# Optimization experiments

Hardware: AMD Instinct MI355X
Metric: run time of the kernel (lower is better)

Reference implementation:

```python
import jax, jax.numpy as jnp
import numpy as np

B, T, D, H, K, V, W = 2, 2048, 1024, 16, 64, 64, 256
BANK = 64
CUE = 50250
EPS = 1e-6
SCALE = K ** -0.5
LOCAL_SCALE = 0.3
ROPE_BASE = 10000.0


def setup_inputs() -> dict:
    key = jax.random.key(0)
    ks = jax.random.split(key, 13)
    s = 0.02
    return {
        "x": jax.random.normal(ks[0], (B, T, D), jnp.float32),
        "gdn_state": jax.random.normal(ks[1], (B, H, K, V), jnp.float32),
        "input_ids": jax.random.randint(ks[2], (B, T), 0, 50320),
        "key_bank": jax.random.normal(ks[3], (H, BANK, K), jnp.float32),
        "norm_w": jnp.ones((D,), jnp.float32),
        "wq": jax.random.normal(ks[4], (D, D), jnp.float32) * s,
        "wk": jax.random.normal(ks[5], (D, D), jnp.float32) * s,
        "wv": jax.random.normal(ks[6], (D, D), jnp.float32) * s,
        "wo": jax.random.normal(ks[7], (D, D), jnp.float32) * s,
        "w_gq": jax.random.normal(ks[8], (H * K, D), jnp.float32) * s,
        "w_ro": jax.random.normal(ks[9], (D, H * V), jnp.float32) * s,
        "w_gate": jax.random.normal(ks[10], (H, D), jnp.float32) * s,
        "b_gate": jnp.ones((H,), jnp.float32),
    }


def _rope(u):
    # u: [B, T, H, K]
    inv_freq = 1.0 / (ROPE_BASE ** (jnp.arange(0, K, 2, dtype=jnp.float32) / K))
    t = jnp.arange(T, dtype=jnp.float32)
    freqs = t[:, None] * inv_freq[None, :]            # [T, K/2]
    emb = jnp.concatenate([freqs, freqs], axis=-1)    # [T, K]
    cos = jnp.cos(emb)[None, :, None, :]
    sin = jnp.sin(emb)[None, :, None, :]
    u1, u2 = u[..., : K // 2], u[..., K // 2 :]
    rotated = jnp.concatenate([-u2, u1], axis=-1)
    return u * cos + rotated * sin


def reference(x, gdn_state, input_ids, key_bank, norm_w, wq, wk, wv, wo,
              w_gq, w_ro, w_gate, b_gate):
    # RMSNorm
    rms = jnp.sqrt(jnp.mean(x * x, axis=-1, keepdims=True) + EPS)
    x_norm = x / rms * norm_w

    # QKV projections -> [B, T, H, K]
    q = (x_norm @ wq.T).reshape(B, T, H, K)
    k = (x_norm @ wk.T).reshape(B, T, H, K)
    v = (x_norm @ wv.T).reshape(B, T, H, K)
    q = _rope(q)
    k = _rope(k)

    # Causal sliding-window attention (PyTorch fallback math: full TxT + band mask)
    scores = jnp.einsum("bthk,bshk->bhts", q, k) * SCALE  # [B, H, T, T]
    i = jnp.arange(T)
    allowed = (i[None, :] <= i[:, None]) & (i[None, :] >= i[:, None] - W)  # [T, T]
    scores = jnp.where(allowed[None, None], scores, jnp.float32(-jnp.inf))
    probs = jax.nn.softmax(scores, axis=-1)
    local = jnp.einsum("bhts,bshv->bthv", probs, v).reshape(B, T, D)
    local = LOCAL_SCALE * (local @ wo.T)  # eval path: local_scale * o_proj(local_out)

    # Global retrieval from GDN state
    q_g = (x_norm @ w_gq.T).reshape(B, T, H, K)
    # CUE token override: positions with input_ids == CUE + idx use key_bank[:, idx, :]
    idx = input_ids - CUE                              # [B, T]
    valid = (idx >= 0) & (idx < BANK)
    ci = jnp.clip(idx, 0, BANK - 1)
    gathered = key_bank.transpose(1, 0, 2)[ci]         # [B, T, H, K]
    q_g = jnp.where(valid[..., None, None], gathered, q_g)

    retrieved = jnp.einsum("bhkv,bthk->bthv", gdn_state, q_g).reshape(B, T, H * V)
    retrieval_out = retrieved @ w_ro.T                 # [B, T, D]
    gate = jax.nn.sigmoid(x_norm @ w_gate.T + b_gate)  # [B, T, H]
    retrieval_out = jnp.mean(gate, axis=-1, keepdims=True) * retrieval_out

    return x + local + retrieval_out
```

## Files before the change

kernel.cpp:

```cpp
#include <hip/hip_runtime.h>
#include <cstddef>

typedef __bf16 bf16_t;
typedef __bf16 bf16x8 __attribute__((ext_vector_type(8)));
typedef __bf16 bf16x4 __attribute__((ext_vector_type(4)));
typedef float  f32x4  __attribute__((ext_vector_type(4)));

struct CvtArgs { const float* s[6]; bf16_t* d[6]; float scale[6]; };
__global__ __launch_bounds__(256) void prep_kernel(CvtArgs ca,
                                                   const float* __restrict__ x,
                                                   const float* __restrict__ nw,
                                                   const float* __restrict__ wg,
                                                   const float* __restrict__ bg,
                                                   bf16_t* __restrict__ xn,
                                                   float* __restrict__ gm,
                                                   float2* __restrict__ rtab,
                                                   float* __restrict__ dout) {
  __shared__ float red[4];
  __shared__ float gred[4][16];
  int bid = blockIdx.x;
  int tid = threadIdx.x;
  if (bid < 6144) {
    int m = bid >> 10;
    int i = (bid & 1023) * 256 + tid;
    f32x4 v = ((const f32x4*)ca.s[m])[i];
    float sc = ca.scale[m];
    bf16x4 o;
    #pragma unroll
    for (int j = 0; j < 4; ++j) o[j] = (bf16_t)(v[j] * sc);
    *(bf16x4*)(ca.d[m] + (size_t)i * 4) = o;
    return;
  }
  if (bid < 6400) {
    int i = (bid - 6144) * 256 + tid;
    int t = i >> 5, d = i & 31;
    float inv = exp2f((float)d * -0.41524101186092029f);
    float sn, cs;
    sincosf((float)t * inv, &sn, &cs);
    rtab[i] = make_float2(cs, sn);
    return;
  }
  int t = bid - 6400;
  int wave = tid >> 6, lane = tid & 63;
  f32x4 v = ((const f32x4*)(x + (size_t)t * 1024))[tid];
  ((f32x4*)(dout + (size_t)t * 1024))[tid] = v;
  float ss = v[0]*v[0] + v[1]*v[1] + v[2]*v[2] + v[3]*v[3];
  #pragma unroll
  for (int off = 32; off >= 1; off >>= 1) ss += __shfl_xor(ss, off);
  if (lane == 0) red[wave] = ss;
  __syncthreads();
  float tot = red[0] + red[1] + red[2] + red[3];
  float rinv = rsqrtf(tot * (1.0f / 1024.0f) + 1e-6f);
  f32x4 wv = ((const f32x4*)nw)[tid];
  float xnv[4];
  bf16x4 o;
  #pragma unroll
  for (int i = 0; i < 4; ++i) { xnv[i] = v[i] * rinv * wv[i]; o[i] = (bf16_t)xnv[i]; }
  *(bf16x4*)(xn + (size_t)t * 1024 + tid * 4) = o;
  float ga[16];
  #pragma unroll
  for (int h = 0; h < 16; ++h) {
    f32x4 wgh = ((const f32x4*)(wg + h * 1024))[tid];
    ga[h] = xnv[0]*wgh[0] + xnv[1]*wgh[1] + xnv[2]*wgh[2] + xnv[3]*wgh[3];
  }
  #pragma unroll
  for (int h = 0; h < 16; ++h) {
    #pragma unroll
    for (int off = 32; off >= 1; off >>= 1) ga[h] += __shfl_xor(ga[h], off);
  }
  if (lane < 16) gred[wave][lane] = ga[lane];
  __syncthreads();
  if (tid < 16) {
    float s = gred[0][tid] + gred[1][tid] + gred[2][tid] + gred[3][tid];
    float sig = 1.0f / (1.0f + __expf(-(s + bg[tid])));
    #pragma unroll
    for (int off = 8; off >= 1; off >>= 1) sig += __shfl_xor(sig, off);
    if (tid == 0) gm[t] = sig * (1.0f / 16.0f);
  }
}

struct GemmSeg { const bf16_t* a; const bf16_t* w; void* c; int mode; };
struct GemmCfg { GemmSeg seg[4]; const float2* rope; };
#define LDSK 40
template<int KD>
__global__ __launch_bounds__(256, 2) void gemm_bt(GemmCfg cfg) {
  __shared__ bf16_t As[128 * LDSK];
  __shared__ bf16_t Bs[128 * LDSK];
  int seg = blockIdx.x >> 3;
  const bf16_t* __restrict__ A = cfg.seg[seg].a;
  const bf16_t* __restrict__ W = cfg.seg[seg].w;
  int m0 = blockIdx.y * 128;
  int n0 = (blockIdx.x & 7) * 128;
  int tid = threadIdx.x;
  int lane = tid & 63, wave = tid >> 6;
  int wm = (wave >> 1) * 64, wn = (wave & 1) * 64;
  int l16 = lane & 15, quad = lane >> 4;
  f32x4 acc[4][4] = {};
  for (int k0 = 0; k0 < KD; k0 += 32) {
    __syncthreads();
    #pragma unroll
    for (int c = 0; c < 2; ++c) {
      int ci = tid + c * 256;
      int r = ci >> 2;
      int ko = (ci & 3) * 8;
      *(uint4*)&As[r * LDSK + ko] = *(const uint4*)&A[(size_t)(m0 + r) * KD + k0 + ko];
      *(uint4*)&Bs[r * LDSK + ko] = *(const uint4*)&W[(size_t)(n0 + r) * KD + k0 + ko];
    }
    __syncthreads();
    bf16x8 af[4], bfr[4];
    #pragma unroll
    for (int i = 0; i < 4; ++i) {
      af[i]  = *(const bf16x8*)&As[(wm + i * 16 + l16) * LDSK + quad * 8];
      bfr[i] = *(const bf16x8*)&Bs[(wn + i * 16 + l16) * LDSK + quad * 8];
    }
    #pragma unroll
    for (int i = 0; i < 4; ++i)
      #pragma unroll
      for (int j = 0; j < 4; ++j)
        acc[i][j] = __builtin_amdgcn_mfma_f32_16x16x32_bf16(af[i], bfr[j], acc[i][j], 0, 0, 0);
  }
  int mode = cfg.seg[seg].mode;
  if (mode == 1) {
    const float2* tab = cfg.rope;
    #pragma unroll
    for (int jp = 0; jp < 2; ++jp) {
      int d = jp * 16 + l16;
      #pragma unroll
      for (int i = 0; i < 4; ++i)
        #pragma unroll
        for (int r = 0; r < 4; ++r) {
          int tseq = (m0 + wm + i * 16 + quad * 4 + r) & 2047;
          float2 cz = tab[(tseq << 5) + d];
          float v1 = acc[i][jp][r], v2 = acc[i][jp + 2][r];
          acc[i][jp][r]     = v1 * cz.x - v2 * cz.y;
          acc[i][jp + 2][r] = v2 * cz.x + v1 * cz.y;
        }
    }
  }
  if (mode == 3) {
    float* C = (float*)cfg.seg[seg].c;
    #pragma unroll
    for (int i = 0; i < 4; ++i)
      #pragma unroll
      for (int j = 0; j < 4; ++j) {
        int row = m0 + wm + i * 16 + quad * 4;
        int col = n0 + wn + j * 16 + l16;
        #pragma unroll
        for (int r = 0; r < 4; ++r)
          unsafeAtomicAdd(&C[(size_t)(row + r) * 1024 + col], acc[i][j][r]);
      }
  } else {
    bf16_t* C = (bf16_t*)cfg.seg[seg].c;
    #pragma unroll
    for (int i = 0; i < 4; ++i)
      #pragma unroll
      for (int j = 0; j < 4; ++j) {
        int row = m0 + wm + i * 16 + quad * 4;
        int col = n0 + wn + j * 16 + l16;
        #pragma unroll
        for (int r = 0; r < 4; ++r)
          C[(size_t)(row + r) * 1024 + col] = (bf16_t)acc[i][j][r];
      }
  }
}

__global__ __launch_bounds__(256) void attn_retr(const bf16_t* __restrict__ qb,
                                                 const bf16_t* __restrict__ kb,
                                                 const bf16_t* __restrict__ vb,
                                                 const bf16_t* __restrict__ qgb,
                                                 const int* __restrict__ ids,
                                                 const float* __restrict__ bank,
                                                 const float* __restrict__ gdn,
                                                 const float* __restrict__ gm,
                                                 bf16_t* __restrict__ attn_b,
                                                 bf16_t* __restrict__ retr_b) {
  __shared__ alignas(16) char smem[35840];
  int tid = threadIdx.x;
  if (blockIdx.x < 1024) {
    bf16_t* Ks = (bf16_t*)smem;
    bf16_t* Vt = (bf16_t*)(smem + 9216);
    float*  Oa = (float*)(smem + 18432);
    int blk = blockIdx.x;
    int tcb = blk & 31;
    int h = (blk >> 5) & 15;
    int b = blk >> 9;
    int t0 = tcb * 64;
    int wv = tid >> 6, lane = tid & 63;
    int l15 = lane & 15, quad = lane >> 4;
    int tq0 = t0 + wv * 16;
    int t = tq0 + l15;
    int lo = t - 256; if (lo < 0) lo = 0;

    const bf16_t* qptr = qb + (((size_t)(b * 2048 + t) * 16) + h) * 64;
    bf16x8 qf0 = *(const bf16x8*)(qptr + quad * 8);
    bf16x8 qf1 = *(const bf16x8*)(qptr + 32 + quad * 8);

    f32x4 acc[4] = {};
    float mrun = -1e30f, lrun = 0.f;

    for (int c = 0; c < 5; ++c) {
      int s0 = t0 - 256 + c * 64;
      __syncthreads();
      #pragma unroll
      for (int it = 0; it < 2; ++it) {
        int task = tid + it * 256;
        int key = task >> 3, dseg = task & 7;
        int s = s0 + key; s = s < 0 ? 0 : (s > 2047 ? 2047 : s);
        *(bf16x8*)&Ks[key * 72 + dseg * 8] =
          *(const bf16x8*)(kb + (((size_t)(b * 2048 + s) * 16) + h) * 64 + dseg * 8);
      }
      {
        int vseg = tid & 7, kp = tid >> 3;
        int sA = s0 + 2 * kp, sB = sA + 1;
        sA = sA < 0 ? 0 : (sA > 2047 ? 2047 : sA);
        sB = sB < 0 ? 0 : (sB > 2047 ? 2047 : sB);
        bf16x8 va = *(const bf16x8*)(vb + (((size_t)(b * 2048 + sA) * 16) + h) * 64 + vseg * 8);
        bf16x8 vbv = *(const bf16x8*)(vb + (((size_t)(b * 2048 + sB) * 16) + h) * 64 + vseg * 8);
        #pragma unroll
        for (int j = 0; j < 8; ++j) {
          union { bf16_t h2[2]; unsigned int u; } pk;
          pk.h2[0] = va[j]; pk.h2[1] = vbv[j];
          *(unsigned int*)&Vt[(vseg * 8 + j) * 72 + 2 * kp] = pk.u;
        }
      }
      __syncthreads();
      #pragma unroll
      for (int p = 0; p < 2; ++p) {
        int sbase = s0 + p * 32;
        if (sbase > tq0 + 15 || sbase + 31 < tq0 - 256 || sbase + 31 < 0) continue;
        int kl = p * 32;
        bf16x8 ka0  = *(const bf16x8*)&Ks[(kl + l15) * 72 + quad * 8];
        bf16x8 ka0b = *(const bf16x8*)&Ks[(kl + l15) * 72 + 32 + quad * 8];
        bf16x8 ka1  = *(const bf16x8*)&Ks[(kl + 16 + l15) * 72 + quad * 8];
        bf16x8 ka1b = *(const bf16x8*)&Ks[(kl + 16 + l15) * 72 + 32 + quad * 8];
        f32x4 c0 = {}, c1 = {};
        c0 = __builtin_amdgcn_mfma_f32_16x16x32_bf16(ka0,  qf0, c0, 0, 0, 0);
        c0 = __builtin_amdgcn_mfma_f32_16x16x32_bf16(ka0b, qf1, c0, 0, 0, 0);
        c1 = __builtin_amdgcn_mfma_f32_16x16x32_bf16(ka1,  qf0, c1, 0, 0, 0);
        c1 = __builtin_amdgcn_mfma_f32_16x16x32_bf16(ka1b, qf1, c1, 0, 0, 0);
        float p0[4], p1[4];
        float mx = -1e30f;
        #pragma unroll
        for (int r = 0; r < 4; ++r) {
          int sK0 = sbase + quad * 4 + r;
          int sK1 = sK0 + 16;
          float v0 = (sK0 >= lo && sK0 <= t) ? c0[r] * 0.125f : -1e30f;
          float v1 = (sK1 >= lo && sK1 <= t) ? c1[r] * 0.125f : -1e30f;
          p0[r] = v0; p1[r] = v1;
          mx = fmaxf(mx, fmaxf(v0, v1));
        }
        mx = fmaxf(mx, __shfl_xor(mx, 16));
        mx = fmaxf(mx, __shfl_xor(mx, 32));
        float mnew = fmaxf(mrun, mx);
        float alpha = __expf(mrun - mnew);
        float rs = 0.f;
        #pragma unroll
        for (int r = 0; r < 4; ++r) {
          float e0 = (p0[r] > -1e29f) ? __expf(p0[r] - mnew) : 0.f;
          float e1 = (p1[r] > -1e29f) ? __expf(p1[r] - mnew) : 0.f;
          p0[r] = e0; p1[r] = e1;
          rs += e0 + e1;
        }
        rs += __shfl_xor(rs, 16);
        rs += __shfl_xor(rs, 32);
        mrun = mnew;
        lrun = lrun * alpha + rs;
        #pragma unroll
        for (int vt = 0; vt < 4; ++vt)
          #pragma unroll
          for (int r = 0; r < 4; ++r) acc[vt][r] *= alpha;
        union { bf16x4 v; int2 i2; } pka, pkb;
        #pragma unroll
        for (int r = 0; r < 4; ++r) { pka.v[r] = (bf16_t)p0[r]; pkb.v[r] = (bf16_t)p1[r]; }
        int sel = quad >> 1;
        int base = l15 + ((quad & 1) << 5);
        int a0 = __shfl(pka.i2.x, base),      b0 = __shfl(pkb.i2.x, base);
        int a1 = __shfl(pka.i2.y, base),      b1 = __shfl(pkb.i2.y, base);
        int a2 = __shfl(pka.i2.x, base + 16), b2 = __shfl(pkb.i2.x, base + 16);
        int a3 = __shfl(pka.i2.y, base + 16), b3 = __shfl(pkb.i2.y, base + 16);
        union { int4 i4; bf16x8 v; } pf;
        pf.i4.x = sel ? b0 : a0;
        pf.i4.y = sel ? b1 : a1;
        pf.i4.z = sel ? b2 : a2;
        pf.i4.w = sel ? b3 : a3;
        #pragma unroll
        for (int vt = 0; vt < 4; ++vt) {
          bf16x8 vfr = *(const bf16x8*)&Vt[(vt * 16 + l15) * 72 + kl + quad * 8];
          acc[vt] = __builtin_amdgcn_mfma_f32_16x16x32_bf16(vfr, pf.v, acc[vt], 0, 0, 0);
        }
      }
    }
    float rl = 1.0f / lrun;
    float* myOs = Oa + wv * (16 * 68);
    #pragma unroll
    for (int vt = 0; vt < 4; ++vt)
      #pragma unroll
      for (int r = 0; r < 4; ++r)
        myOs[l15 * 68 + vt * 16 + quad * 4 + r] = acc[vt][r] * rl;
    __syncthreads();
    #pragma unroll
    for (int q = 0; q < 16; ++q) {
      float v = myOs[q * 68 + lane];
      attn_b[(size_t)(b * 2048 + tq0 + q) * 1024 + h * 64 + lane] = (bf16_t)v;
    }
  } else {
    float* G = (float*)smem;
    int blk = blockIdx.x - 1024;
    int tc = blk & 7;
    int h = (blk >> 3) & 15;
    int b = blk >> 7;
    const f32x4* gsrc = (const f32x4*)(gdn + (size_t)(b * 16 + h) * 4096);
    #pragma unroll
    for (int it = 0; it < 4; ++it)
      ((f32x4*)G)[tid + it * 256] = gsrc[tid + it * 256];
    __syncthreads();
    int t = tc * 256 + tid;
    int id = ids[b * 2048 + t] - 50250;
    bool valid = (id >= 0) && (id < 64);
    const bf16_t* qrow = qgb + (((size_t)(b * 2048 + t) * 16) + h) * 64;
    const float* krow = bank + (size_t)(h * 64 + (valid ? id : 0)) * 64;
    float acc[64];
    #pragma unroll
    for (int v = 0; v < 64; ++v) acc[v] = 0.f;
    for (int k = 0; k < 64; ++k) {
      float qv = valid ? krow[k] : (float)qrow[k];
      const f32x4* gr = (const f32x4*)&G[k * 64];
      #pragma unroll
      for (int i = 0; i < 16; ++i) {
        f32x4 gv = gr[i];
        acc[i * 4 + 0] += qv * gv[0];
        acc[i * 4 + 1] += qv * gv[1];
        acc[i * 4 + 2] += qv * gv[2];
        acc[i * 4 + 3] += qv * gv[3];
      }
    }
    float g = gm[b * 2048 + t];
    bf16_t* orow = retr_b + (size_t)(b * 2048 + t) * 1024 + h * 64;
    #pragma unroll
    for (int i = 0; i < 8; ++i) {
      bf16x8 ov;
      #pragma unroll
      for (int j = 0; j < 8; ++j) ov[j] = (bf16_t)(acc[i * 8 + j] * g);
      *(bf16x8*)(orow + i * 8) = ov;
    }
  }
}

extern "C" void kernel_launch(void* const* d_in, const int* in_sizes, int n_in,
                              void* d_out, int out_size, void* d_ws, size_t ws_size,
                              hipStream_t stream) {
  const float* x        = (const float*)d_in[0];
  const float* gdn      = (const float*)d_in[1];
  const int*   ids      = (const int*)d_in[2];
  const float* key_bank = (const float*)d_in[3];
  const float* norm_w   = (const float*)d_in[4];
  const float* wq       = (const float*)d_in[5];
  const float* wk       = (const float*)d_in[6];
  const float* wv       = (const float*)d_in[7];
  const float* wo       = (const float*)d_in[8];
  const float* w_gq     = (const float*)d_in[9];
  const float* w_ro     = (const float*)d_in[10];
  const float* w_gate   = (const float*)d_in[11];
  const float* b_gate   = (const float*)d_in[12];

  char* p = (char*)d_ws;
  auto alloc = [&](size_t bytes) { char* r = p; p += (bytes + 255) & ~(size_t)255; return r; };
  const size_t ACT = (size_t)4096 * 1024 * 2;
  const size_t WTB = (size_t)1024 * 1024 * 2;
  bf16_t* xn_b   = (bf16_t*)alloc(ACT);
  bf16_t* wq_b   = (bf16_t*)alloc(WTB);
  bf16_t* wk_b   = (bf16_t*)alloc(WTB);
  bf16_t* wv_b   = (bf16_t*)alloc(WTB);
  bf16_t* wgq_b  = (bf16_t*)alloc(WTB);
  bf16_t* wo_b   = (bf16_t*)alloc(WTB);
  bf16_t* wro_b  = (bf16_t*)alloc(WTB);
  bf16_t* qb     = (bf16_t*)alloc(ACT);
  bf16_t* kb     = (bf16_t*)alloc(ACT);
  bf16_t* vb     = (bf16_t*)alloc(ACT);
  bf16_t* qgb    = (bf16_t*)alloc(ACT);
  bf16_t* attn_b = (bf16_t*)alloc(ACT);
  bf16_t* retr_b = (bf16_t*)alloc(ACT);
  float*  gmean  = (float*)alloc(4096 * 4);
  float2* rtab   = (float2*)alloc(2048 * 32 * sizeof(float2));

  CvtArgs ca;
  ca.s[0] = wq;   ca.d[0] = wq_b;   ca.scale[0] = 1.0f;
  ca.s[1] = wk;   ca.d[1] = wk_b;   ca.scale[1] = 1.0f;
  ca.s[2] = wv;   ca.d[2] = wv_b;   ca.scale[2] = 1.0f;
  ca.s[3] = w_gq; ca.d[3] = wgq_b;  ca.scale[3] = 1.0f;
  ca.s[4] = wo;   ca.d[4] = wo_b;   ca.scale[4] = 0.3f;
  ca.s[5] = w_ro; ca.d[5] = wro_b;  ca.scale[5] = 1.0f;
  prep_kernel<<<10496, 256, 0, stream>>>(ca, x, norm_w, w_gate, b_gate,
                                         xn_b, gmean, rtab, (float*)d_out);

  GemmCfg g4;
  g4.seg[0] = {xn_b, wq_b,  (void*)qb,  1};
  g4.seg[1] = {xn_b, wk_b,  (void*)kb,  1};
  g4.seg[2] = {xn_b, wv_b,  (void*)vb,  0};
  g4.seg[3] = {xn_b, wgq_b, (void*)qgb, 0};
  g4.rope = rtab;
  gemm_bt<1024><<<dim3(32, 32), 256, 0, stream>>>(g4);

  attn_retr<<<1280, 256, 0, stream>>>(qb, kb, vb, qgb, ids, key_bank, gdn,
                                      gmean, attn_b, retr_b);

  GemmCfg gf;
  gf.seg[0] = {attn_b, wo_b,  d_out, 3};
  gf.seg[1] = {retr_b, wro_b, d_out, 3};
  gf.seg[2] = gf.seg[0];
  gf.seg[3] = gf.seg[0];
  gf.rope = nullptr;
  gemm_bt<1024><<<dim3(16, 32), 256, 0, stream>>>(gf);
}
```

Before: 263.1 us.

## Split-K the output GEMM and widen K tile for the QKV GEMM

Adds a per-segment K offset so the final output projection is split into two K halves per operand, doubling the grid from 512 to 1024 blocks and relying on mode-3 atomic accumulation into the output. The QKV GEMM switches to a 64-wide K tile, halving the number of barrier pairs per K loop at the cost of more LDS per block. The aim is better CU occupancy on the small output GEMM and less sync overhead on the large one. It adds more atomic traffic and LDS pressure in exchange.

```diff
diff --git a/kernel.cpp b/kernel.cpp
--- a/kernel.cpp
+++ b/kernel.cpp
@@ -79,16 +79,18 @@
   }
 }
 
-struct GemmSeg { const bf16_t* a; const bf16_t* w; void* c; int mode; };
+struct GemmSeg { const bf16_t* a; const bf16_t* w; void* c; int mode; int koff; };
 struct GemmCfg { GemmSeg seg[4]; const float2* rope; };
-#define LDSK 40
-template<int KD>
+template<int KD, int KLEN, int BK>
 __global__ __launch_bounds__(256, 2) void gemm_bt(GemmCfg cfg) {
+  constexpr int LDSK = BK + 8;
+  constexpr int KC = BK / 8;
   __shared__ bf16_t As[128 * LDSK];
   __shared__ bf16_t Bs[128 * LDSK];
   int seg = blockIdx.x >> 3;
   const bf16_t* __restrict__ A = cfg.seg[seg].a;
   const bf16_t* __restrict__ W = cfg.seg[seg].w;
+  int koff = cfg.seg[seg].koff;
   int m0 = blockIdx.y * 128;
   int n0 = (blockIdx.x & 7) * 128;
   int tid = threadIdx.x;
@@ -96,28 +98,31 @@
   int wm = (wave >> 1) * 64, wn = (wave & 1) * 64;
   int l16 = lane & 15, quad = lane >> 4;
   f32x4 acc[4][4] = {};
-  for (int k0 = 0; k0 < KD; k0 += 32) {
+  for (int k0 = koff; k0 < koff + KLEN; k0 += BK) {
     __syncthreads();
     #pragma unroll
-    for (int c = 0; c < 2; ++c) {
+    for (int c = 0; c < BK / 16; ++c) {
       int ci = tid + c * 256;
-      int r = ci >> 2;
-      int ko = (ci & 3) * 8;
+      int r = ci / KC;
+      int ko = (ci % KC) * 8;
       *(uint4*)&As[r * LDSK + ko] = *(const uint4*)&A[(size_t)(m0 + r) * KD + k0 + ko];
       *(uint4*)&Bs[r * LDSK + ko] = *(const uint4*)&W[(size_t)(n0 + r) * KD + k0 + ko];
     }
     __syncthreads();
-    bf16x8 af[4], bfr[4];
-    #pragma unroll
-    for (int i = 0; i < 4; ++i) {
-      af[i]  = *(const bf16x8*)&As[(wm + i * 16 + l16) * LDSK + quad * 8];
-      bfr[i] = *(const bf16x8*)&Bs[(wn + i * 16 + l16) * LDSK + quad * 8];
-    }
-    #pragma unroll
-    for (int i = 0; i < 4; ++i)
-      #pragma unroll
-      for (int j = 0; j < 4; ++j)
-        acc[i][j] = __builtin_amdgcn_mfma_f32_16x16x32_bf16(af[i], bfr[j], acc[i][j], 0, 0, 0);
+    #pragma unroll
+    for (int ks = 0; ks < BK / 32; ++ks) {
+      bf16x8 af[4], bfr[4];
+      #pragma unroll
+      for (int i = 0; i < 4; ++i) {
+        af[i]  = *(const bf16x8*)&As[(wm + i * 16 + l16) * LDSK + ks * 32 + quad * 8];
+        bfr[i] = *(const bf16x8*)&Bs[(wn + i * 16 + l16) * LDSK + ks * 32 + quad * 8];
+      }
+      #pragma unroll
+      for (int i = 0; i < 4; ++i)
+        #pragma unroll
+        for (int j = 0; j < 4; ++j)
+          acc[i][j] = __builtin_amdgcn_mfma_f32_16x16x32_bf16(af[i], bfr[j], acc[i][j], 0, 0, 0);
+    }
   }
   int mode = cfg.seg[seg].mode;
   if (mode == 1) {
@@ -394,21 +399,21 @@
                                          xn_b, gmean, rtab, (float*)d_out);
 
   GemmCfg g4;
-  g4.seg[0] = {xn_b, wq_b,  (void*)qb,  1};
-  g4.seg[1] = {xn_b, wk_b,  (void*)kb,  1};
-  g4.seg[2] = {xn_b, wv_b,  (void*)vb,  0};
-  g4.seg[3] = {xn_b, wgq_b, (void*)qgb, 0};
+  g4.seg[0] = {xn_b, wq_b,  (void*)qb,  1, 0};
+  g4.seg[1] = {xn_b, wk_b,  (void*)kb,  1, 0};
+  g4.seg[2] = {xn_b, wv_b,  (void*)vb,  0, 0};
+  g4.seg[3] = {xn_b, wgq_b, (void*)qgb, 0, 0};
   g4.rope = rtab;
-  gemm_bt<1024><<<dim3(32, 32), 256, 0, stream>>>(g4);
+  gemm_bt<1024, 1024, 64><<<dim3(32, 32), 256, 0, stream>>>(g4);
 
   attn_retr<<<1280, 256, 0, stream>>>(qb, kb, vb, qgb, ids, key_bank, gdn,
                                       gmean, attn_b, retr_b);
 
   GemmCfg gf;
-  gf.seg[0] = {attn_b, wo_b,  d_out, 3};
-  gf.seg[1] = {retr_b, wro_b, d_out, 3};
-  gf.seg[2] = gf.seg[0];
-  gf.seg[3] = gf.seg[0];
+  gf.seg[0] = {attn_b, wo_b,  d_out, 3, 0};
+  gf.seg[1] = {attn_b, wo_b,  d_out, 3, 512};
+  gf.seg[2] = {retr_b, wro_b, d_out, 3, 0};
+  gf.seg[3] = {retr_b, wro_b, d_out, 3, 512};
   gf.rope = nullptr;
-  gemm_bt<1024><<<dim3(16, 32), 256, 0, stream>>>(gf);
+  gemm_bt<1024, 512, 32><<<dim3(32, 32), 256, 0, stream>>>(gf);
 }
```

Measured after the change: 279.4 us. 1.06x slower.

## Chain output GEMM segments along K and add residual in epilogue instead of atomics

Applied to the files above, without the earlier changes.

The final projection GEMM now concatenates the attention and retrieval segments along the K dimension in one block, so each output tile is written once with the residual x added in the epilogue. This replaces fp32 atomic adds and the separate copy of x into the output in the prep kernel. The GEMM also gains register prefetching of the next K-slice from global memory, overlapping loads with MFMA work. In exchange the final GEMM launches half as many blocks (256), each doing twice the K-loop, which lowers parallelism across the CUs.

```diff
diff --git a/kernel.cpp b/kernel.cpp
--- a/kernel.cpp
+++ b/kernel.cpp
@@ -14,8 +14,7 @@
                                                    const float* __restrict__ bg,
                                                    bf16_t* __restrict__ xn,
                                                    float* __restrict__ gm,
-                                                   float2* __restrict__ rtab,
-                                                   float* __restrict__ dout) {
+                                                   float2* __restrict__ rtab) {
   __shared__ float red[4];
   __shared__ float gred[4][16];
   int bid = blockIdx.x;
@@ -43,7 +42,6 @@
   int t = bid - 6400;
   int wave = tid >> 6, lane = tid & 63;
   f32x4 v = ((const f32x4*)(x + (size_t)t * 1024))[tid];
-  ((f32x4*)(dout + (size_t)t * 1024))[tid] = v;
   float ss = v[0]*v[0] + v[1]*v[1] + v[2]*v[2] + v[3]*v[3];
   #pragma unroll
   for (int off = 32; off >= 1; off >>= 1) ss += __shfl_xor(ss, off);
@@ -80,33 +78,41 @@
 }
 
 struct GemmSeg { const bf16_t* a; const bf16_t* w; void* c; int mode; };
-struct GemmCfg { GemmSeg seg[4]; const float2* rope; };
+struct GemmCfg { GemmSeg seg[4]; const float2* rope; const float* x; };
 #define LDSK 40
-template<int KD>
+template<int NPH>
 __global__ __launch_bounds__(256, 2) void gemm_bt(GemmCfg cfg) {
   __shared__ bf16_t As[128 * LDSK];
   __shared__ bf16_t Bs[128 * LDSK];
-  int seg = blockIdx.x >> 3;
-  const bf16_t* __restrict__ A = cfg.seg[seg].a;
-  const bf16_t* __restrict__ W = cfg.seg[seg].w;
+  const GemmSeg* sp = &cfg.seg[(blockIdx.x >> 3) * NPH];
   int m0 = blockIdx.y * 128;
   int n0 = (blockIdx.x & 7) * 128;
   int tid = threadIdx.x;
   int lane = tid & 63, wave = tid >> 6;
   int wm = (wave >> 1) * 64, wn = (wave & 1) * 64;
   int l16 = lane & 15, quad = lane >> 4;
+  int ci0 = tid, ci1 = tid + 256;
+  int r0 = ci0 >> 2, k0o = (ci0 & 3) * 8;
+  int r1 = ci1 >> 2, k1o = (ci1 & 3) * 8;
+  uint4 pa0, pa1, pb0, pb1;
+  auto prefetch = [&](const bf16_t* A_, const bf16_t* W_, int k0) {
+    pa0 = *(const uint4*)&A_[(size_t)(m0 + r0) * 1024 + k0 + k0o];
+    pa1 = *(const uint4*)&A_[(size_t)(m0 + r1) * 1024 + k0 + k1o];
+    pb0 = *(const uint4*)&W_[(size_t)(n0 + r0) * 1024 + k0 + k0o];
+    pb1 = *(const uint4*)&W_[(size_t)(n0 + r1) * 1024 + k0 + k1o];
+  };
   f32x4 acc[4][4] = {};
-  for (int k0 = 0; k0 < KD; k0 += 32) {
+  prefetch(sp[0].a, sp[0].w, 0);
+  for (int kk = 0; kk < NPH * 1024; kk += 32) {
     __syncthreads();
-    #pragma unroll
-    for (int c = 0; c < 2; ++c) {
-      int ci = tid + c * 256;
-      int r = ci >> 2;
-      int ko = (ci & 3) * 8;
-      *(uint4*)&As[r * LDSK + ko] = *(const uint4*)&A[(size_t)(m0 + r) * KD + k0 + ko];
-      *(uint4*)&Bs[r * LDSK + ko] = *(const uint4*)&W[(size_t)(n0 + r) * KD + k0 + ko];
-    }
+    *(uint4*)&As[r0 * LDSK + k0o] = pa0;
+    *(uint4*)&As[r1 * LDSK + k1o] = pa1;
+    *(uint4*)&Bs[r0 * LDSK + k0o] = pb0;
+    *(uint4*)&Bs[r1 * LDSK + k1o] = pb1;
     __syncthreads();
+    int kn = kk + 32;
+    if (kn < NPH * 1024)
+      prefetch(sp[kn >> 10].a, sp[kn >> 10].w, kn & 1023);
     bf16x8 af[4], bfr[4];
     #pragma unroll
     for (int i = 0; i < 4; ++i) {
@@ -119,7 +125,7 @@
       for (int j = 0; j < 4; ++j)
         acc[i][j] = __builtin_amdgcn_mfma_f32_16x16x32_bf16(af[i], bfr[j], acc[i][j], 0, 0, 0);
   }
-  int mode = cfg.seg[seg].mode;
+  int mode = sp[0].mode;
   if (mode == 1) {
     const float2* tab = cfg.rope;
     #pragma unroll
@@ -137,8 +143,9 @@
         }
     }
   }
-  if (mode == 3) {
-    float* C = (float*)cfg.seg[seg].c;
+  if (mode == 2) {
+    float* C = (float*)sp[0].c;
+    const float* X = cfg.x;
     #pragma unroll
     for (int i = 0; i < 4; ++i)
       #pragma unroll
@@ -146,11 +153,13 @@
         int row = m0 + wm + i * 16 + quad * 4;
         int col = n0 + wn + j * 16 + l16;
         #pragma unroll
-        for (int r = 0; r < 4; ++r)
-          unsafeAtomicAdd(&C[(size_t)(row + r) * 1024 + col], acc[i][j][r]);
+        for (int r = 0; r < 4; ++r) {
+          size_t idx = (size_t)(row + r) * 1024 + col;
+          C[idx] = X[idx] + acc[i][j][r];
+        }
       }
   } else {
-    bf16_t* C = (bf16_t*)cfg.seg[seg].c;
+    bf16_t* C = (bf16_t*)sp[0].c;
     #pragma unroll
     for (int i = 0; i < 4; ++i)
       #pragma unroll
@@ -391,7 +400,7 @@
   ca.s[4] = wo;   ca.d[4] = wo_b;   ca.scale[4] = 0.3f;
   ca.s[5] = w_ro; ca.d[5] = wro_b;  ca.scale[5] = 1.0f;
   prep_kernel<<<10496, 256, 0, stream>>>(ca, x, norm_w, w_gate, b_gate,
-                                         xn_b, gmean, rtab, (float*)d_out);
+                                         xn_b, gmean, rtab);
 
   GemmCfg g4;
   g4.seg[0] = {xn_b, wq_b,  (void*)qb,  1};
@@ -399,16 +408,16 @@
   g4.seg[2] = {xn_b, wv_b,  (void*)vb,  0};
   g4.seg[3] = {xn_b, wgq_b, (void*)qgb, 0};
   g4.rope = rtab;
-  gemm_bt<1024><<<dim3(32, 32), 256, 0, stream>>>(g4);
+  g4.x = nullptr;
+  gemm_bt<1><<<dim3(32, 32), 256, 0, stream>>>(g4);
 
   attn_retr<<<1280, 256, 0, stream>>>(qb, kb, vb, qgb, ids, key_bank, gdn,
                                       gmean, attn_b, retr_b);
 
   GemmCfg gf;
-  gf.seg[0] = {attn_b, wo_b,  d_out, 3};
-  gf.seg[1] = {retr_b, wro_b, d_out, 3};
-  gf.seg[2] = gf.seg[0];
-  gf.seg[3] = gf.seg[0];
+  gf.seg[0] = {attn_b, wo_b,  d_out, 2};
+  gf.seg[1] = {retr_b, wro_b, d_out, 2};
   gf.rope = nullptr;
-  gemm_bt<1024><<<dim3(16, 32), 256, 0, stream>>>(gf);
+  gf.x = x;
+  gemm_bt<2><<<dim3(8, 32), 256, 0, stream>>>(gf);
 }
```

After: 262.0 us. About the same (-0.4%).
